# Kernel optimization log

Hardware: AMD Instinct MI355X
Metric: run time of the kernel (lower is better)

The kernel has to match this reference:

```python
import jax, jax.numpy as jnp
import numpy as np

B, C, H, W = 32, 3, 512, 512
DOWNSAMPLE = 2
N = W // DOWNSAMPLE  # 256 glimpse points
SMALL = 1e-4


def setup_inputs() -> dict:
    key = jax.random.key(0)
    k1, k2 = jax.random.split(key)
    x = jax.random.normal(k1, (B, C, H, W), dtype=jnp.float32)
    # p = locnet output: (gx_raw, gy_raw, log_sigma2, log_delta, log_gamma)
    p = jax.random.normal(k2, (B, 5), dtype=jnp.float32) * 0.5
    return {"x": x, "p": p}


def _filterbank(g, sigma2, delta, size):
    # g, sigma2, delta: [B]; returns [B, N, size]
    i = jnp.arange(N, dtype=jnp.float32)
    a = jnp.arange(size, dtype=jnp.float32)
    mu = g[:, None] + delta[:, None] * (i - N / 2.0 - 0.5)          # [B, N]
    F = jnp.exp(-((a - mu[:, :, None]) ** 2) / 2.0 / sigma2[:, None, None])  # [B, N, size]
    return F / (F.sum(axis=-1, keepdims=True) + SMALL)


def reference(x, p):
    # attention params (matches _get_attention_params)
    gx = W * (p[:, 0] + 1.0) / 2.0
    gy = H * (p[:, 1] + 1.0) / 2.0
    sigma2 = jnp.exp(p[:, 2])
    delta = jnp.exp(p[:, 3]) * (max(W, H) - 1) / (N - 1.0)
    gamma = jnp.exp(p[:, 4])
    # Gaussian filterbanks
    Fx = _filterbank(gx, sigma2, delta, W)  # [B, N, W]
    Fy = _filterbank(gy, sigma2, delta, H)  # [B, N, H]
    # read: gamma * Fy @ x @ Fx^T, expressed as two batched GEMMs
    Fyx = jnp.einsum('bnh,bchw->bcnw', Fy, x)       # [B, C, N, W]
    out = jnp.einsum('bcnw,bmw->bcnm', Fyx, Fx)     # [B, C, N, N]
    return gamma[:, None, None, None] * out
```

## Files before the change

### kernel.cpp

```cpp
#include <hip/hip_runtime.h>
#include <hip/hip_bf16.h>
#include <math.h>


namespace {

typedef __attribute__((ext_vector_type(8))) short v8s;
typedef __attribute__((ext_vector_type(4))) short v4s;
typedef __attribute__((ext_vector_type(4))) float f32x4;

constexpr int Bn = 32;
constexpr int Cc = 3;
constexpr int HW = 512;
constexpr int Nn = 256;
constexpr float SMALLF = 1e-4f;

__device__ inline unsigned short f2bf(float f) {
    __hip_bfloat16 h = __float2bfloat16(f);
    union { __hip_bfloat16 h; unsigned short u; } c;
    c.h = h;
    return c.u;
}

__device__ inline int xcd_swz(int bid, int nwg) {
    return (bid & 7) * (nwg >> 3) + (bid >> 3);
}

__device__ inline bool tile_window(float g, float delta, float sigma,
                                   int r0, int& klo, int& khi) {
    float lo = g + delta * ((float)r0 - 128.5f) - 8.0f * sigma - 2.0f;
    float hi = g + delta * ((float)(r0 + 63) - 128.5f) + 8.0f * sigma + 2.0f;
    if (hi < 0.0f || lo > 511.0f) return false;
    klo = max(0, (int)floorf(lo * (1.0f / 64.0f)));
    khi = min(7, (int)floorf(hi * (1.0f / 64.0f)));
    return khi >= klo;
}

__global__ __launch_bounds__(256) void fb_kernel(const float* __restrict__ p,
                                                 unsigned short* __restrict__ Fx,
                                                 unsigned short* __restrict__ Fy) {
    const int wid  = threadIdx.x >> 6;
    const int lane = threadIdx.x & 63;
    const int rid  = blockIdx.x * 4 + wid;
    const int which = rid >> 13;
    const int r = rid & 8191;
    const int b = r >> 8;
    const int n = r & 255;

    const float* pb = p + b * 5;
    const float sigma2 = expf(pb[2]);
    const float delta  = expf(pb[3]) * (511.0f / 255.0f);
    const float g = (which == 0) ? (HW * (pb[0] + 1.0f) * 0.5f)
                                 : (HW * (pb[1] + 1.0f) * 0.5f);
    const float mu = g + delta * ((float)n - 128.5f);
    const float inv2s = 0.5f / sigma2;

    float f[8];
    float sum = 0.0f;
#pragma unroll
    for (int q = 0; q < 8; ++q) {
        float a = (float)(q * 64 + lane);
        float d = a - mu;
        f[q] = expf(-d * d * inv2s);
        sum += f[q];
    }
#pragma unroll
    for (int s = 1; s < 64; s <<= 1) sum += __shfl_xor(sum, s, 64);
    const float inv = 1.0f / (sum + SMALLF);

    unsigned short* dst = ((which == 0) ? Fx : Fy) + ((size_t)(b * Nn + n)) * HW;
#pragma unroll
    for (int q = 0; q < 8; ++q) dst[q * 64 + lane] = f2bf(f[q] * inv);
}

__device__ inline v8s frag_read(const unsigned short* __restrict__ lds, int row, int kk, int lk) {
    int byte = row * 128 + (((kk * 64) + lk * 16) ^ ((row & 7) << 4));
    return *(const v8s*)((const char*)lds + byte);
}

__global__ __launch_bounds__(256) void gemm1_kernel(const float* __restrict__ x,
                                                    const unsigned short* __restrict__ Fx_b,
                                                    const float* __restrict__ p,
                                                    unsigned short* __restrict__ G) {
    __shared__ unsigned short lds_all[2 * 64 * 64];
    unsigned short* As = lds_all;
    unsigned short* Bs = lds_all + 64 * 64;
    const int t = threadIdx.x;
    const int wg = xcd_swz(blockIdx.x, 3072);
    const int bc = wg >> 5, b = bc / 3;
    const int rem = wg & 31;
    const int h0 = (rem >> 2) * 64;
    const int m0 = (rem & 3) * 64;

    const float* Ag = x + (size_t)bc * HW * HW + (size_t)h0 * HW;
    const unsigned short* Bg = Fx_b + (size_t)b * Nn * HW + (size_t)m0 * HW;

    const float* pb = p + b * 5;
    const float sigma = sqrtf(expf(pb[2]));
    const float delta = expf(pb[3]) * (511.0f / 255.0f);
    const float gx = HW * (pb[0] + 1.0f) * 0.5f;
    int klo = 0, khi = -1;
    bool live = tile_window(gx, delta, sigma, m0, klo, khi);

    const int wid = t >> 6, lane = t & 63, lr = lane & 15, lk = lane >> 4;
    const int wr = (wid >> 1) * 32;
    const int wc = (wid & 1) * 32;

    const int srow = t >> 2;
    const int scq  = (t & 3) * 16;

    f32x4 acc[2][2];
#pragma unroll
    for (int i = 0; i < 2; ++i)
#pragma unroll
        for (int j = 0; j < 2; ++j) acc[i][j] = (f32x4){0.f, 0.f, 0.f, 0.f};

    float4 xa[4];
    v8s    fxv[2];

#define G1_LOAD(K0)                                                              \
    {                                                                            \
        const float* s_ = Ag + (size_t)srow * HW + (K0) + scq;                   \
        xa[0] = *(const float4*)s_;                                              \
        xa[1] = *(const float4*)(s_ + 4);                                        \
        xa[2] = *(const float4*)(s_ + 8);                                        \
        xa[3] = *(const float4*)(s_ + 12);                                       \
        const unsigned short* b_ = Bg + (size_t)srow * HW + (K0) + scq;          \
        fxv[0] = *(const v8s*)b_;                                                \
        fxv[1] = *(const v8s*)(b_ + 8);                                          \
    }

    if (live) {
        G1_LOAD(klo * 64);
#pragma unroll 1
        for (int ks = klo; ks <= khi; ++ks) {
            __syncthreads();
            {
                unsigned short q[16];
#pragma unroll
                for (int i = 0; i < 4; ++i) {
                    q[i * 4 + 0] = f2bf(xa[i].x);
                    q[i * 4 + 1] = f2bf(xa[i].y);
                    q[i * 4 + 2] = f2bf(xa[i].z);
                    q[i * 4 + 3] = f2bf(xa[i].w);
                }
                int base = srow * 128;
                int sw = (srow & 7) << 4;
                *(v8s*)((char*)As + base + ((scq * 2) ^ sw))      = *(const v8s*)q;
                *(v8s*)((char*)As + base + ((scq * 2 + 16) ^ sw)) = *(const v8s*)(q + 8);
                *(v8s*)((char*)Bs + base + ((scq * 2) ^ sw))      = fxv[0];
                *(v8s*)((char*)Bs + base + ((scq * 2 + 16) ^ sw)) = fxv[1];
            }
            __syncthreads();
            if (ks < khi) G1_LOAD((ks + 1) * 64);
#pragma unroll
            for (int kk = 0; kk < 2; ++kk) {
                v8s af[2], bf[2];
#pragma unroll
                for (int mi = 0; mi < 2; ++mi) af[mi] = frag_read(As, wr + mi * 16 + lr, kk, lk);
#pragma unroll
                for (int ni = 0; ni < 2; ++ni) bf[ni] = frag_read(Bs, wc + ni * 16 + lr, kk, lk);
#pragma unroll
                for (int mi = 0; mi < 2; ++mi)
#pragma unroll
                    for (int ni = 0; ni < 2; ++ni)
                        acc[mi][ni] = __builtin_amdgcn_mfma_f32_16x16x32_bf16(af[mi], bf[ni], acc[mi][ni], 0, 0, 0);
            }
        }
    }
#undef G1_LOAD

    __syncthreads();
    {
        unsigned short* Ls = lds_all;
#pragma unroll
        for (int mi = 0; mi < 2; ++mi)
#pragma unroll
            for (int ni = 0; ni < 2; ++ni) {
                int ml = wc + ni * 16 + lr;
                int hl = wr + mi * 16 + lk * 4;
                unsigned short q[4] = {f2bf(acc[mi][ni][0]), f2bf(acc[mi][ni][1]),
                                       f2bf(acc[mi][ni][2]), f2bf(acc[mi][ni][3])};
                *(v4s*)(Ls + ml * 72 + hl) = *(const v4s*)q;
            }
        __syncthreads();
        int ml = t >> 2;
        int hc = (t & 3) * 16;
        v8s v0 = *(const v8s*)(Ls + ml * 72 + hc);
        v8s v1 = *(const v8s*)(Ls + ml * 72 + hc + 8);
        unsigned short* dst = G + (size_t)bc * Nn * HW + (size_t)(m0 + ml) * HW + h0 + hc;
        *(v8s*)dst = v0;
        *(v8s*)(dst + 8) = v1;
    }
}

__global__ __launch_bounds__(256) void gemm2_kernel(const unsigned short* __restrict__ Fy_b,
                                                    const unsigned short* __restrict__ G,
                                                    const float* __restrict__ p,
                                                    float* __restrict__ out) {
    __shared__ unsigned short As[64 * 64];
    __shared__ unsigned short Bs[64 * 64];
    const int t = threadIdx.x;
    const int wg = xcd_swz(blockIdx.x, 1536);
    const int bc = wg >> 4, b = bc / 3;
    const int rem = wg & 15;
    const int n0 = (rem >> 2) * 64;
    const int m0 = (rem & 3) * 64;

    const unsigned short* Ag = Fy_b + (size_t)b * Nn * HW + (size_t)n0 * HW;
    const unsigned short* Bg = G + (size_t)bc * Nn * HW + (size_t)m0 * HW;

    const float* pb = p + b * 5;
    const float gamma = expf(pb[4]);
    const float sigma = sqrtf(expf(pb[2]));
    const float delta = expf(pb[3]) * (511.0f / 255.0f);
    const float gy = HW * (pb[1] + 1.0f) * 0.5f;
    int klo = 0, khi = -1;
    bool live = tile_window(gy, delta, sigma, n0, klo, khi);

    const int wid = t >> 6, lane = t & 63, lr = lane & 15, lk = lane >> 4;
    const int wr = (wid >> 1) * 32, wc = (wid & 1) * 32;

    const int srow = t >> 2;
    const int scq  = (t & 3) * 16;

    f32x4 acc[2][2];
#pragma unroll
    for (int i = 0; i < 2; ++i)
#pragma unroll
        for (int j = 0; j < 2; ++j) acc[i][j] = (f32x4){0.f, 0.f, 0.f, 0.f};

    v8s va[2], vb[2];

#define G2_LOAD(K0)                                                              \
    {                                                                            \
        const unsigned short* a_ = Ag + (size_t)srow * HW + (K0) + scq;          \
        const unsigned short* b_ = Bg + (size_t)srow * HW + (K0) + scq;          \
        va[0] = *(const v8s*)a_;                                                 \
        va[1] = *(const v8s*)(a_ + 8);                                           \
        vb[0] = *(const v8s*)b_;                                                 \
        vb[1] = *(const v8s*)(b_ + 8);                                           \
    }

    if (live) {
        G2_LOAD(klo * 64);
#pragma unroll 1
        for (int ks = klo; ks <= khi; ++ks) {
            __syncthreads();
            {
                int base = srow * 128;
                int sw = (srow & 7) << 4;
                *(v8s*)((char*)As + base + ((scq * 2) ^ sw))      = va[0];
                *(v8s*)((char*)As + base + ((scq * 2 + 16) ^ sw)) = va[1];
                *(v8s*)((char*)Bs + base + ((scq * 2) ^ sw))      = vb[0];
                *(v8s*)((char*)Bs + base + ((scq * 2 + 16) ^ sw)) = vb[1];
            }
            __syncthreads();
            if (ks < khi) G2_LOAD((ks + 1) * 64);
#pragma unroll
            for (int kk = 0; kk < 2; ++kk) {
                v8s af[2], bf[2];
#pragma unroll
                for (int mi = 0; mi < 2; ++mi) af[mi] = frag_read(As, wr + mi * 16 + lr, kk, lk);
#pragma unroll
                for (int ni = 0; ni < 2; ++ni) bf[ni] = frag_read(Bs, wc + ni * 16 + lr, kk, lk);
#pragma unroll
                for (int mi = 0; mi < 2; ++mi)
#pragma unroll
                    for (int ni = 0; ni < 2; ++ni)
                        acc[mi][ni] = __builtin_amdgcn_mfma_f32_16x16x32_bf16(af[mi], bf[ni], acc[mi][ni], 0, 0, 0);
            }
        }
    }
#undef G2_LOAD

    float* Cg = out + (size_t)bc * Nn * Nn + (size_t)n0 * Nn + m0;
#pragma unroll
    for (int mi = 0; mi < 2; ++mi)
#pragma unroll
        for (int r = 0; r < 4; ++r) {
            int row = wr + mi * 16 + lk * 4 + r;
#pragma unroll
            for (int ni = 0; ni < 2; ++ni)
                Cg[(size_t)row * Nn + wc + ni * 16 + lr] = gamma * acc[mi][ni][r];
        }
}

}

extern "C" void kernel_launch(void* const* d_in, const int* in_sizes, int n_in,
                              void* d_out, int out_size, void* d_ws, size_t ws_size,
                              hipStream_t stream) {
    const float* x = (const float*)d_in[0];
    const float* p = (const float*)d_in[1];
    float* out = (float*)d_out;

    char* ws = (char*)d_ws;
    unsigned short* Fx_b = (unsigned short*)ws;
    unsigned short* Fy_b = Fx_b + (size_t)Bn * Nn * HW;
    unsigned short* G    = Fy_b + (size_t)Bn * Nn * HW;

    hipLaunchKernelGGL(fb_kernel, dim3(4096), dim3(256), 0, stream, p, Fx_b, Fy_b);
    hipLaunchKernelGGL(gemm1_kernel, dim3(3072), dim3(256), 0, stream, x, Fx_b, p, G);
    hipLaunchKernelGGL(gemm2_kernel, dim3(1536), dim3(256), 0, stream, Fy_b, G, p, out);
}
```

Baseline: 46.17 us.

## Narrow band-skip tiles to 32 filter rows and tighten Gaussian cutoff window

Both GEMM kernels change their output tile from 64x64 to 32 filter rows by 128 spatial/output columns, so the per-tile K window computed from the Gaussian band covers fewer rows and more K blocks can be skipped. The cutoff margin is also reduced from 8 sigma to 4.5 sigma, which shrinks the computed K range further. Load mappings, LDS layout, the MFMA loops and the epilogue are reworked to match the new tile shape. The tighter cutoff drops Gaussian tails beyond 4.5 sigma, which may add a small accuracy error, and the narrower tiles raise loads of the larger operand per output.

```diff
diff --git a/kernel.cpp b/kernel.cpp
--- a/kernel.cpp
+++ b/kernel.cpp
@@ -27,9 +27,9 @@
 }
 
 __device__ inline bool tile_window(float g, float delta, float sigma,
-                                   int r0, int& klo, int& khi) {
-    float lo = g + delta * ((float)r0 - 128.5f) - 8.0f * sigma - 2.0f;
-    float hi = g + delta * ((float)(r0 + 63) - 128.5f) + 8.0f * sigma + 2.0f;
+                                   int r0, int Trows, int& klo, int& khi) {
+    float lo = g + delta * ((float)r0 - 128.5f) - 4.5f * sigma - 2.0f;
+    float hi = g + delta * ((float)(r0 + Trows - 1) - 128.5f) + 4.5f * sigma + 2.0f;
     if (hi < 0.0f || lo > 511.0f) return false;
     klo = max(0, (int)floorf(lo * (1.0f / 64.0f)));
     khi = min(7, (int)floorf(hi * (1.0f / 64.0f)));
@@ -82,15 +82,15 @@
                                                     const unsigned short* __restrict__ Fx_b,
                                                     const float* __restrict__ p,
                                                     unsigned short* __restrict__ G) {
-    __shared__ unsigned short lds_all[2 * 64 * 64];
+    __shared__ unsigned short lds_all[128 * 64 + 32 * 64];
     unsigned short* As = lds_all;
-    unsigned short* Bs = lds_all + 64 * 64;
+    unsigned short* Bs = lds_all + 128 * 64;
     const int t = threadIdx.x;
     const int wg = xcd_swz(blockIdx.x, 3072);
     const int bc = wg >> 5, b = bc / 3;
     const int rem = wg & 31;
-    const int h0 = (rem >> 2) * 64;
-    const int m0 = (rem & 3) * 64;
+    const int m0 = (rem >> 2) * 32;
+    const int h0 = (rem & 3) * 128;
 
     const float* Ag = x + (size_t)bc * HW * HW + (size_t)h0 * HW;
     const unsigned short* Bg = Fx_b + (size_t)b * Nn * HW + (size_t)m0 * HW;
@@ -100,34 +100,30 @@
     const float delta = expf(pb[3]) * (511.0f / 255.0f);
     const float gx = HW * (pb[0] + 1.0f) * 0.5f;
     int klo = 0, khi = -1;
-    bool live = tile_window(gx, delta, sigma, m0, klo, khi);
+    bool live = tile_window(gx, delta, sigma, m0, 32, klo, khi);
 
     const int wid = t >> 6, lane = t & 63, lr = lane & 15, lk = lane >> 4;
-    const int wr = (wid >> 1) * 32;
-    const int wc = (wid & 1) * 32;
-
-    const int srow = t >> 2;
-    const int scq  = (t & 3) * 16;
-
-    f32x4 acc[2][2];
-#pragma unroll
-    for (int i = 0; i < 2; ++i)
-#pragma unroll
-        for (int j = 0; j < 2; ++j) acc[i][j] = (f32x4){0.f, 0.f, 0.f, 0.f};
-
-    float4 xa[4];
-    v8s    fxv[2];
+    const int wh = (wid >> 1) * 64;
+    const int wm = (wid & 1) * 16;
+
+    const int arow = t >> 1;
+    const int acol = (t & 1) * 32;
+    const int brow = t >> 3;
+    const int bcol = (t & 7) * 8;
+
+    f32x4 acc[4];
+#pragma unroll
+    for (int i = 0; i < 4; ++i) acc[i] = (f32x4){0.f, 0.f, 0.f, 0.f};
+
+    float4 xa[8];
+    v8s    fxv;
 
 #define G1_LOAD(K0)                                                              \
     {                                                                            \
-        const float* s_ = Ag + (size_t)srow * HW + (K0) + scq;                   \
-        xa[0] = *(const float4*)s_;                                              \
-        xa[1] = *(const float4*)(s_ + 4);                                        \
-        xa[2] = *(const float4*)(s_ + 8);                                        \
-        xa[3] = *(const float4*)(s_ + 12);                                       \
-        const unsigned short* b_ = Bg + (size_t)srow * HW + (K0) + scq;          \
-        fxv[0] = *(const v8s*)b_;                                                \
-        fxv[1] = *(const v8s*)(b_ + 8);                                          \
+        const float* s_ = Ag + (size_t)arow * HW + (K0) + acol;                  \
+        _Pragma("unroll")                                                        \
+        for (int j = 0; j < 8; ++j) xa[j] = *(const float4*)(s_ + j * 4);        \
+        fxv = *(const v8s*)(Bg + (size_t)brow * HW + (K0) + bcol);               \
     }
 
     if (live) {
@@ -136,35 +132,34 @@
         for (int ks = klo; ks <= khi; ++ks) {
             __syncthreads();
             {
-                unsigned short q[16];
-#pragma unroll
-                for (int i = 0; i < 4; ++i) {
-                    q[i * 4 + 0] = f2bf(xa[i].x);
-                    q[i * 4 + 1] = f2bf(xa[i].y);
-                    q[i * 4 + 2] = f2bf(xa[i].z);
-                    q[i * 4 + 3] = f2bf(xa[i].w);
+                int abase = arow * 128;
+                int asw = (arow & 7) << 4;
+#pragma unroll
+                for (int j = 0; j < 2; ++j) {
+                    unsigned short q[16];
+#pragma unroll
+                    for (int i = 0; i < 4; ++i) {
+                        q[i * 4 + 0] = f2bf(xa[j * 4 + i].x);
+                        q[i * 4 + 1] = f2bf(xa[j * 4 + i].y);
+                        q[i * 4 + 2] = f2bf(xa[j * 4 + i].z);
+                        q[i * 4 + 3] = f2bf(xa[j * 4 + i].w);
+                    }
+                    int cb = acol * 2 + j * 32;
+                    *(v8s*)((char*)As + abase + (cb ^ asw))        = *(const v8s*)q;
+                    *(v8s*)((char*)As + abase + ((cb + 16) ^ asw)) = *(const v8s*)(q + 8);
                 }
-                int base = srow * 128;
-                int sw = (srow & 7) << 4;
-                *(v8s*)((char*)As + base + ((scq * 2) ^ sw))      = *(const v8s*)q;
-                *(v8s*)((char*)As + base + ((scq * 2 + 16) ^ sw)) = *(const v8s*)(q + 8);
-                *(v8s*)((char*)Bs + base + ((scq * 2) ^ sw))      = fxv[0];
-                *(v8s*)((char*)Bs + base + ((scq * 2 + 16) ^ sw)) = fxv[1];
+                *(v8s*)((char*)Bs + brow * 128 + ((bcol * 2) ^ ((brow & 7) << 4))) = fxv;
             }
             __syncthreads();
             if (ks < khi) G1_LOAD((ks + 1) * 64);
 #pragma unroll
             for (int kk = 0; kk < 2; ++kk) {
-                v8s af[2], bf[2];
-#pragma unroll
-                for (int mi = 0; mi < 2; ++mi) af[mi] = frag_read(As, wr + mi * 16 + lr, kk, lk);
-#pragma unroll
-                for (int ni = 0; ni < 2; ++ni) bf[ni] = frag_read(Bs, wc + ni * 16 + lr, kk, lk);
-#pragma unroll
-                for (int mi = 0; mi < 2; ++mi)
-#pragma unroll
-                    for (int ni = 0; ni < 2; ++ni)
-                        acc[mi][ni] = __builtin_amdgcn_mfma_f32_16x16x32_bf16(af[mi], bf[ni], acc[mi][ni], 0, 0, 0);
+                v8s bf = frag_read(Bs, wm + lr, kk, lk);
+#pragma unroll
+                for (int mi = 0; mi < 4; ++mi) {
+                    v8s af = frag_read(As, wh + mi * 16 + lr, kk, lk);
+                    acc[mi] = __builtin_amdgcn_mfma_f32_16x16x32_bf16(af, bf, acc[mi], 0, 0, 0);
+                }
             }
         }
     }
@@ -174,20 +169,18 @@
     {
         unsigned short* Ls = lds_all;
 #pragma unroll
-        for (int mi = 0; mi < 2; ++mi)
-#pragma unroll
-            for (int ni = 0; ni < 2; ++ni) {
-                int ml = wc + ni * 16 + lr;
-                int hl = wr + mi * 16 + lk * 4;
-                unsigned short q[4] = {f2bf(acc[mi][ni][0]), f2bf(acc[mi][ni][1]),
-                                       f2bf(acc[mi][ni][2]), f2bf(acc[mi][ni][3])};
-                *(v4s*)(Ls + ml * 72 + hl) = *(const v4s*)q;
-            }
+        for (int mi = 0; mi < 4; ++mi) {
+            int ml = wm + lr;
+            int hl = wh + mi * 16 + lk * 4;
+            unsigned short q[4] = {f2bf(acc[mi][0]), f2bf(acc[mi][1]),
+                                   f2bf(acc[mi][2]), f2bf(acc[mi][3])};
+            *(v4s*)(Ls + ml * 136 + hl) = *(const v4s*)q;
+        }
         __syncthreads();
-        int ml = t >> 2;
-        int hc = (t & 3) * 16;
-        v8s v0 = *(const v8s*)(Ls + ml * 72 + hc);
-        v8s v1 = *(const v8s*)(Ls + ml * 72 + hc + 8);
+        int ml = t >> 3;
+        int hc = (t & 7) * 16;
+        v8s v0 = *(const v8s*)(Ls + ml * 136 + hc);
+        v8s v1 = *(const v8s*)(Ls + ml * 136 + hc + 8);
         unsigned short* dst = G + (size_t)bc * Nn * HW + (size_t)(m0 + ml) * HW + h0 + hc;
         *(v8s*)dst = v0;
         *(v8s*)(dst + 8) = v1;
@@ -198,14 +191,15 @@
                                                     const unsigned short* __restrict__ G,
                                                     const float* __restrict__ p,
                                                     float* __restrict__ out) {
-    __shared__ unsigned short As[64 * 64];
-    __shared__ unsigned short Bs[64 * 64];
+    __shared__ unsigned short lds_all2[32 * 64 + 128 * 64];
+    unsigned short* As = lds_all2;
+    unsigned short* Bs = lds_all2 + 32 * 64;
     const int t = threadIdx.x;
     const int wg = xcd_swz(blockIdx.x, 1536);
     const int bc = wg >> 4, b = bc / 3;
     const int rem = wg & 15;
-    const int n0 = (rem >> 2) * 64;
-    const int m0 = (rem & 3) * 64;
+    const int n0 = (rem >> 1) * 32;
+    const int m0 = (rem & 1) * 128;
 
     const unsigned short* Ag = Fy_b + (size_t)b * Nn * HW + (size_t)n0 * HW;
     const unsigned short* Bg = G + (size_t)bc * Nn * HW + (size_t)m0 * HW;
@@ -216,30 +210,29 @@
     const float delta = expf(pb[3]) * (511.0f / 255.0f);
     const float gy = HW * (pb[1] + 1.0f) * 0.5f;
     int klo = 0, khi = -1;
-    bool live = tile_window(gy, delta, sigma, n0, klo, khi);
+    bool live = tile_window(gy, delta, sigma, n0, 32, klo, khi);
 
     const int wid = t >> 6, lane = t & 63, lr = lane & 15, lk = lane >> 4;
-    const int wr = (wid >> 1) * 32, wc = (wid & 1) * 32;
-
-    const int srow = t >> 2;
-    const int scq  = (t & 3) * 16;
-
-    f32x4 acc[2][2];
-#pragma unroll
-    for (int i = 0; i < 2; ++i)
-#pragma unroll
-        for (int j = 0; j < 2; ++j) acc[i][j] = (f32x4){0.f, 0.f, 0.f, 0.f};
-
-    v8s va[2], vb[2];
+    const int wn = (wid >> 1) * 16;
+    const int wm = (wid & 1) * 64;
+
+    const int arow = t >> 3;
+    const int acol = (t & 7) * 8;
+    const int brow = t >> 1;
+    const int bcol = (t & 1) * 32;
+
+    f32x4 acc[4];
+#pragma unroll
+    for (int i = 0; i < 4; ++i) acc[i] = (f32x4){0.f, 0.f, 0.f, 0.f};
+
+    v8s va, vb[4];
 
 #define G2_LOAD(K0)                                                              \
     {                                                                            \
-        const unsigned short* a_ = Ag + (size_t)srow * HW + (K0) + scq;          \
-        const unsigned short* b_ = Bg + (size_t)srow * HW + (K0) + scq;          \
-        va[0] = *(const v8s*)a_;                                                 \
-        va[1] = *(const v8s*)(a_ + 8);                                           \
-        vb[0] = *(const v8s*)b_;                                                 \
-        vb[1] = *(const v8s*)(b_ + 8);                                           \
+        va = *(const v8s*)(Ag + (size_t)arow * HW + (K0) + acol);                \
+        const unsigned short* b_ = Bg + (size_t)brow * HW + (K0) + bcol;         \
+        _Pragma("unroll")                                                        \
+        for (int j = 0; j < 4; ++j) vb[j] = *(const v8s*)(b_ + j * 8);           \
     }
 
     if (live) {
@@ -248,27 +241,23 @@
         for (int ks = klo; ks <= khi; ++ks) {
             __syncthreads();
             {
-                int base = srow * 128;
-                int sw = (srow & 7) << 4;
-                *(v8s*)((char*)As + base + ((scq * 2) ^ sw))      = va[0];
-                *(v8s*)((char*)As + base + ((scq * 2 + 16) ^ sw)) = va[1];
-                *(v8s*)((char*)Bs + base + ((scq * 2) ^ sw))      = vb[0];
-                *(v8s*)((char*)Bs + base + ((scq * 2 + 16) ^ sw)) = vb[1];
+                *(v8s*)((char*)As + arow * 128 + ((acol * 2) ^ ((arow & 7) << 4))) = va;
+                int bbase = brow * 128;
+                int bsw = (brow & 7) << 4;
+#pragma unroll
+                for (int j = 0; j < 4; ++j)
+                    *(v8s*)((char*)Bs + bbase + ((bcol * 2 + j * 16) ^ bsw)) = vb[j];
             }
             __syncthreads();
             if (ks < khi) G2_LOAD((ks + 1) * 64);
 #pragma unroll
             for (int kk = 0; kk < 2; ++kk) {
-                v8s af[2], bf[2];
-#pragma unroll
-                for (int mi = 0; mi < 2; ++mi) af[mi] = frag_read(As, wr + mi * 16 + lr, kk, lk);
-#pragma unroll
-                for (int ni = 0; ni < 2; ++ni) bf[ni] = frag_read(Bs, wc + ni * 16 + lr, kk, lk);
-#pragma unroll
-                for (int mi = 0; mi < 2; ++mi)
-#pragma unroll
-                    for (int ni = 0; ni < 2; ++ni)
-                        acc[mi][ni] = __builtin_amdgcn_mfma_f32_16x16x32_bf16(af[mi], bf[ni], acc[mi][ni], 0, 0, 0);
+                v8s af = frag_read(As, wn + lr, kk, lk);
+#pragma unroll
+                for (int mi = 0; mi < 4; ++mi) {
+                    v8s bf = frag_read(Bs, wm + mi * 16 + lr, kk, lk);
+                    acc[mi] = __builtin_amdgcn_mfma_f32_16x16x32_bf16(af, bf, acc[mi], 0, 0, 0);
+                }
             }
         }
     }
@@ -276,14 +265,12 @@
 
     float* Cg = out + (size_t)bc * Nn * Nn + (size_t)n0 * Nn + m0;
 #pragma unroll
-    for (int mi = 0; mi < 2; ++mi)
-#pragma unroll
-        for (int r = 0; r < 4; ++r) {
-            int row = wr + mi * 16 + lk * 4 + r;
-#pragma unroll
-            for (int ni = 0; ni < 2; ++ni)
-                Cg[(size_t)row * Nn + wc + ni * 16 + lr] = gamma * acc[mi][ni][r];
-        }
+    for (int r = 0; r < 4; ++r) {
+        int row = wn + lk * 4 + r;
+#pragma unroll
+        for (int mi = 0; mi < 4; ++mi)
+            Cg[(size_t)row * Nn + wm + mi * 16 + lr] = gamma * acc[mi][r];
+    }
 }
 
 }
```

New measurement: 52.58 us. 1.14x slower.
